# Kernel tuning notes

Measured on AMD Instinct MI355X. Metric: run time of the kernel, lower is better.

The kernel has to match this reference:

```python
import jax, jax.numpy as jnp
import numpy as np

B, L0, L1, NS, D, H, NL, HM = 16, 512, 256, 32, 256, 8, 4, 4
T = L0 + L1 + NS + 1
HD = D // H
EPS = 1e-5
SCALE = HD ** -0.5


def setup_inputs() -> dict:
    key = jax.random.key(0)
    ks = jax.random.split(key, 20)
    s = 0.02
    return {
        'seq_tokens_0': jax.random.normal(ks[0], (B, L0, D), jnp.float32),
        'seq_tokens_1': jax.random.normal(ks[1], (B, L1, D), jnp.float32),
        'seq_lens_0': jax.random.randint(ks[2], (B,), 0, L0),
        'seq_lens_1': jax.random.randint(ks[3], (B,), 0, L1),
        'ns_tokens': jax.random.normal(ks[4], (B, NS, D), jnp.float32),
        'domain_emb': jax.random.normal(ks[5], (2, D), jnp.float32) * s,
        'cls_token': jax.random.normal(ks[6], (1, 1, D), jnp.float32) * s,
        'ln1_w': jnp.ones((NL, D), jnp.float32),
        'ln1_b': jnp.zeros((NL, D), jnp.float32),
        'qkv_w': jax.random.normal(ks[7], (NL, D, 3 * D), jnp.float32) * s,
        'qkv_b': jnp.zeros((NL, 3 * D), jnp.float32),
        'out_w': jax.random.normal(ks[8], (NL, D, D), jnp.float32) * s,
        'out_b': jnp.zeros((NL, D), jnp.float32),
        'ln2_w': jnp.ones((NL, D), jnp.float32),
        'ln2_b': jnp.zeros((NL, D), jnp.float32),
        'ffn1_w': jax.random.normal(ks[9], (NL, D, HM * D), jnp.float32) * s,
        'ffn1_b': jnp.zeros((NL, HM * D), jnp.float32),
        'ffn2_w': jax.random.normal(ks[10], (NL, HM * D, D), jnp.float32) * s,
        'ffn2_b': jnp.zeros((NL, D), jnp.float32),
        'fln_w': jnp.ones((D,), jnp.float32),
        'fln_b': jnp.zeros((D,), jnp.float32),
    }


def _ln(x, w, b):
    m = jnp.mean(x, -1, keepdims=True)
    v = jnp.var(x, -1, keepdims=True)
    return (x - m) * jax.lax.rsqrt(v + EPS) * w + b


def _build_mask(seq_lens_0, seq_lens_1):
    # static block structure: intra-domain causal, S<->NS bidirectional, CLS sink row
    base = jnp.zeros((T, T), bool)
    base = base.at[:L0, :L0].set(jnp.tril(jnp.ones((L0, L0), bool)))
    base = base.at[L0:L0 + L1, L0:L0 + L1].set(jnp.tril(jnp.ones((L1, L1), bool)))
    ns_s, ns_e = L0 + L1, L0 + L1 + NS
    base = base.at[:ns_s, ns_s:ns_e].set(True)   # S -> NS
    base = base.at[ns_s:ns_e, :ns_e].set(True)   # NS -> S and NS -> NS
    base = base.at[T - 1, :ns_e].set(True)       # CLS reads all S/NS
    base = base.at[T - 1, T - 1].set(True)       # CLS reads itself
    # per-batch padding mask on keys of each seq segment
    kv = jnp.ones((B, T), bool)
    kv = kv.at[:, :L0].set(jnp.arange(L0)[None, :] < seq_lens_0[:, None])
    kv = kv.at[:, L0:L0 + L1].set(jnp.arange(L1)[None, :] < seq_lens_1[:, None])
    return base[None] & kv[:, None, :]  # [B, T, T]


def _attention(x, mask, qkv_w, qkv_b, out_w, out_b):
    qkv = (x @ qkv_w + qkv_b).reshape(B, T, 3, H, HD)
    q, k, v = qkv[:, :, 0], qkv[:, :, 1], qkv[:, :, 2]
    scores = jnp.einsum('bqhd,bkhd->bhqk', q, k) * SCALE
    m = mask[:, None]  # [B,1,T,T]
    s = jnp.where(m, scores, -jnp.inf)
    any_valid = jnp.any(m, -1, keepdims=True)
    mx = jnp.where(any_valid, jnp.max(s, -1, keepdims=True), 0.0)
    e = jnp.exp(s - mx)  # masked entries exp(-inf)=0
    denom = jnp.sum(e, -1, keepdims=True)
    probs = e / jnp.maximum(denom, 1e-30)  # fully-masked rows -> zeros
    out = jnp.einsum('bhqk,bkhd->bqhd', probs, v).reshape(B, T, D)
    return out @ out_w + out_b


def reference(seq_tokens_0, seq_tokens_1, seq_lens_0, seq_lens_1, ns_tokens,
              domain_emb, cls_token, ln1_w, ln1_b, qkv_w, qkv_b, out_w, out_b,
              ln2_w, ln2_b, ffn1_w, ffn1_b, ffn2_w, ffn2_b, fln_w, fln_b):
    t0 = seq_tokens_0 + domain_emb[0][None, None, :]
    t1 = seq_tokens_1 + domain_emb[1][None, None, :]
    cls = jnp.broadcast_to(cls_token, (B, 1, D))
    x = jnp.concatenate([t0, t1, ns_tokens, cls], axis=1)  # [B,T,D]
    mask = _build_mask(seq_lens_0, seq_lens_1)
    for l in range(NL):
        x = x + _attention(_ln(x, ln1_w[l], ln1_b[l]), mask,
                           qkv_w[l], qkv_b[l], out_w[l], out_b[l])
        h = _ln(x, ln2_w[l], ln2_b[l])
        h = jax.nn.gelu(h @ ffn1_w[l] + ffn1_b[l], approximate=False)
        x = x + h @ ffn2_w[l] + ffn2_b[l]
    x = _ln(x, fln_w, fln_b)
    return x[:, -1, :]  # CLS state [B,D]
```

## Files before the change

kernel.cpp:

```cpp
#include <hip/hip_runtime.h>
#include <hip/hip_bf16.h>
#include <math.h>

typedef __attribute__((ext_vector_type(8))) unsigned short ushort8;
typedef __attribute__((ext_vector_type(8))) short short8;
typedef __attribute__((ext_vector_type(4))) float f32x4;
typedef __attribute__((ext_vector_type(4))) unsigned short ushort4v;
typedef __attribute__((ext_vector_type(4))) int i32x4;
typedef unsigned int u32;

namespace {
constexpr int B = 16, L0 = 512, L1 = 256, NS = 32, D = 256, H = 8, NL = 4, HM = 4;
constexpr int T = L0 + L1 + NS + 1;
constexpr int HD = D / H;
constexpr int NTOK = B * T;
constexpr int NS_S = L0 + L1;
constexpr int NS_E = NS_S + NS;
constexpr int TPAD = 832;
constexpr float EPS = 1e-5f;
constexpr float SCL2  = 0.17677669529663687f * 1.4426950408889634f;
}

__device__ __forceinline__ ushort f2bf(float f) {
    union { float f; unsigned u; } v; v.f = f;
    return (ushort)((v.u + 0x7fffu + ((v.u >> 16) & 1u)) >> 16);
}

__device__ __forceinline__ u32 cvtpk(float a, float b) {
    u32 r;
    asm("v_cvt_pk_bf16_f32 %0, %1, %2" : "=v"(r) : "v"(a), "v"(b));
    return r;
}

__device__ __forceinline__ void gload_lds16(const void* g, void* l) {
    __builtin_amdgcn_global_load_lds(
        (const __attribute__((address_space(1))) u32*)g,
        (__attribute__((address_space(3))) u32*)l, 16, 0, 0);
}

__global__ __launch_bounds__(256) void k_wprep(
    const float* __restrict__ src, ushort* __restrict__ dst, int K, int N)
{
    const size_t off = (size_t)blockIdx.z * K * N;
    src += off; dst += off;
    __shared__ float t[32][33];
    const int kb = blockIdx.x * 32, nb = blockIdx.y * 32;
    const int c = threadIdx.x & 31, r8 = threadIdx.x >> 5;
#pragma unroll
    for (int rr = 0; rr < 32; rr += 8)
        t[r8 + rr][c] = src[(size_t)(kb + r8 + rr) * N + nb + c];
    __syncthreads();
#pragma unroll
    for (int rr = 0; rr < 32; rr += 8)
        dst[(size_t)(nb + r8 + rr) * K + kb + c] = f2bf(t[c][r8 + rr]);
}

__global__ __launch_bounds__(256) void k_build_ln(
    const float* __restrict__ s0, const float* __restrict__ s1,
    const float* __restrict__ ns, const float* __restrict__ dom,
    const float* __restrict__ cls, const float* __restrict__ lnw,
    const float* __restrict__ lnb, float* __restrict__ x, ushort* __restrict__ xn)
{
    const int wid = threadIdx.x >> 6, lane = threadIdx.x & 63;
    const int row = blockIdx.x * 4 + wid;
    if (row >= NTOK) return;
    const int b = row / T, t = row % T;
    const int d0 = lane * 4;
    float4 v;
    if (t < L0) {
        v = *(const float4*)(s0 + ((size_t)b * L0 + t) * D + d0);
        float4 dm = *(const float4*)(dom + d0);
        v.x += dm.x; v.y += dm.y; v.z += dm.z; v.w += dm.w;
    } else if (t < NS_S) {
        v = *(const float4*)(s1 + ((size_t)b * L1 + (t - L0)) * D + d0);
        float4 dm = *(const float4*)(dom + D + d0);
        v.x += dm.x; v.y += dm.y; v.z += dm.z; v.w += dm.w;
    } else if (t < NS_E) {
        v = *(const float4*)(ns + ((size_t)b * NS + (t - NS_S)) * D + d0);
    } else {
        v = *(const float4*)(cls + d0);
    }
    *(float4*)(x + (size_t)row * D + d0) = v;
    float s  = v.x + v.y + v.z + v.w;
    float ss = v.x * v.x + v.y * v.y + v.z * v.z + v.w * v.w;
#pragma unroll
    for (int o = 32; o; o >>= 1) { s += __shfl_xor(s, o); ss += __shfl_xor(ss, o); }
    const float mean = s * (1.f / D);
    const float var  = ss * (1.f / D) - mean * mean;
    const float r = rsqrtf(var + EPS);
    float4 wv = *(const float4*)(lnw + d0);
    float4 bv = *(const float4*)(lnb + d0);
    ushort4v o4;
    o4[0] = f2bf((v.x - mean) * r * wv.x + bv.x);
    o4[1] = f2bf((v.y - mean) * r * wv.y + bv.y);
    o4[2] = f2bf((v.z - mean) * r * wv.z + bv.z);
    o4[3] = f2bf((v.w - mean) * r * wv.w + bv.w);
    *(ushort4v*)(xn + (size_t)row * D + d0) = o4;
}

template<bool GELU, bool RES, bool OBF, bool CLSW>
__global__ __launch_bounds__(256) void k_gemm_mfma(
    const ushort* __restrict__ A, const ushort* __restrict__ Wt,
    const float* __restrict__ bias, void* __restrict__ Cout,
    const float* __restrict__ res, int M, int N, int K)
{
    __shared__ ushort As[2][128 * 64];
    __shared__ ushort Bs[2][128 * 64];
    const int tid = threadIdx.x;
    const int lane = tid & 63, w = tid >> 6;
    const int lo = lane & 15, g = lane >> 4;
    const int wr = w >> 1, wc = w & 1;
    const int m0 = CLSW ? (((blockIdx.x * T + (T - 1)) >> 7) << 7) : blockIdx.x * 128;
    const int n0 = blockIdx.y * 128;

    f32x4 zero = {0.f, 0.f, 0.f, 0.f};
    f32x4 acc[4][4];
#pragma unroll
    for (int mi = 0; mi < 4; ++mi)
#pragma unroll
        for (int ni = 0; ni < 4; ++ni) acc[mi][ni] = zero;

    const ushort* srcA[4];
    const ushort* srcB[4];
    int ldsOff[4];
#pragma unroll
    for (int i = 0; i < 4; ++i) {
        const int idx16 = (w * 4 + i) * 64 + lane;
        const int row = idx16 >> 3;
        const int scb = ((idx16 & 7) * 16) ^ ((row & 7) << 4);
        int arow = m0 + row; if (arow >= M) arow = M - 1;
        srcA[i] = A  + (size_t)arow * K + (scb >> 1);
        srcB[i] = Wt + (size_t)(n0 + row) * K + (scb >> 1);
        ldsOff[i] = (w * 4 + i) * 512;
    }

    const int NT = K >> 6;
#pragma unroll
    for (int i = 0; i < 4; ++i) {
        gload_lds16(srcA[i], &As[0][ldsOff[i]]);
        gload_lds16(srcB[i], &Bs[0][ldsOff[i]]);
    }
    asm volatile("s_waitcnt vmcnt(0)");
    __syncthreads();

    for (int t = 0; t < NT; ++t) {
        const int buf = t & 1;
        if (t + 1 < NT) {
            const int nb = buf ^ 1, ko = (t + 1) * 64;
#pragma unroll
            for (int i = 0; i < 4; ++i) {
                gload_lds16(srcA[i] + ko, &As[nb][ldsOff[i]]);
                gload_lds16(srcB[i] + ko, &Bs[nb][ldsOff[i]]);
            }
        }
#pragma unroll
        for (int kk = 0; kk < 2; ++kk) {
            const int kb = (kk * 64 + g * 16) ^ ((lo & 7) << 4);
            short8 af[4], bfr[4];
#pragma unroll
            for (int mi = 0; mi < 4; ++mi)
                af[mi] = *(const short8*)&As[buf][(wr * 64 + mi * 16 + lo) * 64 + (kb >> 1)];
#pragma unroll
            for (int ni = 0; ni < 4; ++ni)
                bfr[ni] = *(const short8*)&Bs[buf][(wc * 64 + ni * 16 + lo) * 64 + (kb >> 1)];
#pragma unroll
            for (int mi = 0; mi < 4; ++mi)
#pragma unroll
                for (int ni = 0; ni < 4; ++ni)
                    acc[mi][ni] = __builtin_amdgcn_mfma_f32_16x16x32_bf16(
                        af[mi], bfr[ni], acc[mi][ni], 0, 0, 0);
        }
        asm volatile("s_waitcnt vmcnt(0)");
        __syncthreads();
    }

    float bv[4];
#pragma unroll
    for (int ni = 0; ni < 4; ++ni) bv[ni] = bias[n0 + wc * 64 + ni * 16 + lo];
#pragma unroll
    for (int mi = 0; mi < 4; ++mi) {
#pragma unroll
        for (int i = 0; i < 4; ++i) {
            const int row = m0 + wr * 64 + mi * 16 + g * 4 + i;
            if (row >= M) continue;
#pragma unroll
            for (int ni = 0; ni < 4; ++ni) {
                const int col = n0 + wc * 64 + ni * 16 + lo;
                float v = acc[mi][ni][i] + bv[ni];
                if (GELU) v = 0.5f * v * (1.0f + erff(v * 0.70710678118654752f));
                if (RES)  v += res[(size_t)row * N + col];
                if (OBF) ((ushort*)Cout)[(size_t)row * N + col] = f2bf(v);
                else     ((float*)Cout)[(size_t)row * N + col] = v;
            }
        }
    }
}

template<int MODE, bool CLSW>
__global__ __launch_bounds__(256) void k_gemm_fused(
    const ushort* __restrict__ A, const ushort* __restrict__ Wt,
    const float* __restrict__ bias, const float* __restrict__ res,
    const float* __restrict__ lnw, const float* __restrict__ lnb,
    float* __restrict__ xout, ushort* __restrict__ xnout,
    float* __restrict__ dout, int M, int K)
{
    __shared__ ushort As[2][64 * 64];
    __shared__ ushort Bs[2][256 * 64];
    __shared__ float redS[64][4];
    __shared__ float redQ[64][4];
    const int tid = threadIdx.x;
    const int lane = tid & 63, w = tid >> 6;
    const int lo = lane & 15, g = lane >> 4;
    const int m0 = CLSW ? (((blockIdx.x * T + (T - 1)) >> 6) << 6) : blockIdx.x * 64;

    f32x4 zero = {0.f, 0.f, 0.f, 0.f};
    f32x4 acc[4][4];
#pragma unroll
    for (int mi = 0; mi < 4; ++mi)
#pragma unroll
        for (int ni = 0; ni < 4; ++ni) acc[mi][ni] = zero;

    const ushort* srcA[2]; int ldsOffA[2];
    const ushort* srcB[8]; int ldsOffB[8];
#pragma unroll
    for (int j = 0; j < 2; ++j) {
        const int idx16 = j * 256 + tid;
        const int row = idx16 >> 3;
        const int scb = ((idx16 & 7) * 16) ^ ((row & 7) << 4);
        int arow = m0 + row; if (arow >= M) arow = M - 1;
        srcA[j] = A + (size_t)arow * K + (scb >> 1);
        ldsOffA[j] = idx16 * 8;
    }
#pragma unroll
    for (int j = 0; j < 8; ++j) {
        const int idx16 = j * 256 + tid;
        const int row = idx16 >> 3;
        const int scb = ((idx16 & 7) * 16) ^ ((row & 7) << 4);
        srcB[j] = Wt + (size_t)row * K + (scb >> 1);
        ldsOffB[j] = idx16 * 8;
    }

    const int NT = K >> 6;
#pragma unroll
    for (int j = 0; j < 2; ++j) gload_lds16(srcA[j], &As[0][ldsOffA[j]]);
#pragma unroll
    for (int j = 0; j < 8; ++j) gload_lds16(srcB[j], &Bs[0][ldsOffB[j]]);
    asm volatile("s_waitcnt vmcnt(0)");
    __syncthreads();

    for (int t = 0; t < NT; ++t) {
        const int buf = t & 1;
        if (t + 1 < NT) {
            const int nb = buf ^ 1, ko = (t + 1) * 64;
#pragma unroll
            for (int j = 0; j < 2; ++j) gload_lds16(srcA[j] + ko, &As[nb][ldsOffA[j]]);
#pragma unroll
            for (int j = 0; j < 8; ++j) gload_lds16(srcB[j] + ko, &Bs[nb][ldsOffB[j]]);
        }
#pragma unroll
        for (int kk = 0; kk < 2; ++kk) {
            const int kb = (kk * 64 + g * 16) ^ ((lo & 7) << 4);
            short8 af[4], bfr[4];
#pragma unroll
            for (int mi = 0; mi < 4; ++mi)
                af[mi] = *(const short8*)&As[buf][(mi * 16 + lo) * 64 + (kb >> 1)];
#pragma unroll
            for (int ni = 0; ni < 4; ++ni)
                bfr[ni] = *(const short8*)&Bs[buf][(w * 64 + ni * 16 + lo) * 64 + (kb >> 1)];
#pragma unroll
            for (int mi = 0; mi < 4; ++mi)
#pragma unroll
                for (int ni = 0; ni < 4; ++ni)
                    acc[mi][ni] = __builtin_amdgcn_mfma_f32_16x16x32_bf16(
                        af[mi], bfr[ni], acc[mi][ni], 0, 0, 0);
        }
        asm volatile("s_waitcnt vmcnt(0)");
        __syncthreads();
    }

    float bv[4], lw[4], lb[4];
#pragma unroll
    for (int ni = 0; ni < 4; ++ni) {
        const int c = w * 64 + ni * 16 + lo;
        bv[ni] = bias[c]; lw[ni] = lnw[c]; lb[ni] = lnb[c];
    }
#pragma unroll
    for (int mi = 0; mi < 4; ++mi) {
#pragma unroll
        for (int i = 0; i < 4; ++i) {
            const int r64 = mi * 16 + g * 4 + i;
            const int row = m0 + r64;
            float s = 0.f, q = 0.f;
            if (row < M) {
#pragma unroll
                for (int ni = 0; ni < 4; ++ni) {
                    const int col = w * 64 + ni * 16 + lo;
                    float v = acc[mi][ni][i] + bv[ni] + res[(size_t)row * 256 + col];
                    acc[mi][ni][i] = v;
                    s += v; q += v * v;
                }
                s += __shfl_xor(s, 1); q += __shfl_xor(q, 1);
                s += __shfl_xor(s, 2); q += __shfl_xor(q, 2);
                s += __shfl_xor(s, 4); q += __shfl_xor(q, 4);
                s += __shfl_xor(s, 8); q += __shfl_xor(q, 8);
                if (lo == 0) { redS[r64][w] = s; redQ[r64][w] = q; }
            }
        }
    }
    __syncthreads();
#pragma unroll
    for (int mi = 0; mi < 4; ++mi) {
#pragma unroll
        for (int i = 0; i < 4; ++i) {
            const int r64 = mi * 16 + g * 4 + i;
            const int row = m0 + r64;
            if (row >= M) continue;
            const float S = redS[r64][0] + redS[r64][1] + redS[r64][2] + redS[r64][3];
            const float Q = redQ[r64][0] + redQ[r64][1] + redQ[r64][2] + redQ[r64][3];
            const float mean = S * (1.f / 256.f);
            const float var  = Q * (1.f / 256.f) - mean * mean;
            const float rstd = rsqrtf(var + EPS);
            if (MODE == 0) {
#pragma unroll
                for (int ni = 0; ni < 4; ++ni) {
                    const int col = w * 64 + ni * 16 + lo;
                    const float v = acc[mi][ni][i];
                    xout[(size_t)row * 256 + col] = v;
                    xnout[(size_t)row * 256 + col] = f2bf((v - mean) * rstd * lw[ni] + lb[ni]);
                }
            } else {
                const int bq = row / T;
                const int tq = row - bq * T;
                if (tq == T - 1) {
#pragma unroll
                    for (int ni = 0; ni < 4; ++ni) {
                        const int col = w * 64 + ni * 16 + lo;
                        dout[(size_t)bq * 256 + col] =
                            (acc[mi][ni][i] - mean) * rstd * lw[ni] + lb[ni];
                    }
                }
            }
        }
    }
}

__global__ __launch_bounds__(256) void k_repack(
    const ushort* __restrict__ qkv, ushort* __restrict__ Kb, ushort* __restrict__ Vt)
{
    const int bh = blockIdx.x, tt = blockIdx.y;
    const int b = bh >> 3, h = bh & 7;
    const int tid = threadIdx.x;
    const int r = tid >> 2, c = tid & 3;
    const int t = tt * 64 + r;
    __shared__ ushort vtile[64][40];
    ushort8 k8 = {0,0,0,0,0,0,0,0}, v8 = {0,0,0,0,0,0,0,0};
    if (t < T) {
        const ushort* kp = qkv + ((size_t)(b * T + t) * 3 + 1) * D + h * HD + c * 8;
        k8 = *(const ushort8*)kp;
        v8 = *(const ushort8*)(kp + D);
    }
    *(ushort8*)(Kb + ((size_t)bh * TPAD + tt * 64 + r) * HD + c * 8) = k8;
    *(ushort8*)&vtile[r][c * 8] = v8;
    __syncthreads();
    const int d = tid >> 3, cc = tid & 7;
    ushort8 o;
#pragma unroll
    for (int j = 0; j < 8; ++j) o[j] = vtile[cc * 8 + j][d];
    *(ushort8*)(Vt + ((size_t)bh * HD + d) * TPAD + tt * 64 + cc * 8) = o;
}

__global__ __launch_bounds__(256) void k_flash(
    const ushort* __restrict__ qkv, const ushort* __restrict__ Kb,
    const ushort* __restrict__ Vt, const int* __restrict__ len0,
    const int* __restrict__ len1, ushort* __restrict__ out)
{
    const int bh = blockIdx.x;
    const int qt = 12 - blockIdx.y;
    const int b = bh >> 3, h = bh & 7;
    const int tid = threadIdx.x, lane = tid & 63, w = tid >> 6;
    const int lo = lane & 15, g = lane >> 4;
    const int b4 = g & 1, b5 = g >> 1;
    const int q = qt * 64 + w * 16 + lo;
    const int l0b = len0[b], lim01 = L0 + len1[b];

    int klo = 0, klim;
    if (q < L0)        klim = q;
    else if (q < NS_S) { klo = L0; klim = q; }
    else if (q < NS_E) klim = NS_E - 1;
    else               klim = q;

    int qrow = q; if (qrow > T - 1) qrow = T - 1;
    short8 qf = *(const short8*)(qkv + ((size_t)(b * T + qrow) * 3) * D + h * HD + g * 8);

    const ushort* Kbase = Kb + (size_t)bh * TPAD * HD;
    const ushort* Vbase = Vt + (size_t)bh * HD * TPAD;

    f32x4 acc0 = {0.f, 0.f, 0.f, 0.f}, acc1 = {0.f, 0.f, 0.f, 0.f};
    float mrow = -1e30f, srow = 0.f;

    const int kts = (qt >= 8 && qt < 12) ? 8 : 0;
    const int ntiles = (qt < 12) ? (qt - kts + 2) : 13;
    auto ktile = [&](int it) { int kt = kts + it; return kt > qt ? 12 : kt; };

    short8 kf[4];
    {
        const int k0 = ktile(0) * 64;
#pragma unroll
        for (int n = 0; n < 4; ++n)
            kf[n] = *(const short8*)(Kbase + (size_t)(k0 + n * 16 + lo) * HD + g * 8);
    }

    for (int it = 0; it < ntiles; ++it) {
        const int k0 = ktile(it) * 64;

        const ushort* V0 = Vbase + k0;
        short8 a00 = *(const short8*)(V0 + (size_t)lo * TPAD + g * 8);
        short8 a01 = *(const short8*)(V0 + (size_t)lo * TPAD + 32 + g * 8);
        short8 a10 = *(const short8*)(V0 + (size_t)(16 + lo) * TPAD + g * 8);
        short8 a11 = *(const short8*)(V0 + (size_t)(16 + lo) * TPAD + 32 + g * 8);

        float pv[4][4];
        float tmax = -1e30f;
#pragma unroll
        for (int n = 0; n < 4; ++n) {
            f32x4 z = {0.f, 0.f, 0.f, 0.f};
            f32x4 sn = __builtin_amdgcn_mfma_f32_16x16x32_bf16(kf[n], qf, z, 0, 0, 0);
#pragma unroll
            for (int i = 0; i < 4; ++i) {
                const int k = k0 + n * 16 + g * 4 + i;
                const bool inNS = (k >= NS_S) & (k < NS_E);
                const bool kval = (k < l0b) | ((k >= L0) & (k < lim01)) | (k >= NS_S);
                const bool m = ((k >= klo) & (k <= klim) & kval) | inNS;
                const float sv = m ? sn[i] * SCL2 : -1e30f;
                pv[n][i] = sv;
                tmax = fmaxf(tmax, sv);
            }
        }

        short8 kf2[4];
        if (it + 1 < ntiles) {
            const int k1 = ktile(it + 1) * 64;
#pragma unroll
            for (int n = 0; n < 4; ++n)
                kf2[n] = *(const short8*)(Kbase + (size_t)(k1 + n * 16 + lo) * HD + g * 8);
        }

        tmax = fmaxf(tmax, __shfl_xor(tmax, 16));
        tmax = fmaxf(tmax, __shfl_xor(tmax, 32));
        const float mnew = fmaxf(mrow, tmax);
        const float scl = exp2f(mrow - mnew);
        mrow = mnew;

        u32 C0[4], C1[4];
        float psum = 0.f;
#pragma unroll
        for (int n = 0; n < 4; ++n) {
            float e0 = exp2f(pv[n][0] - mnew);
            float e1 = exp2f(pv[n][1] - mnew);
            float e2 = exp2f(pv[n][2] - mnew);
            float e3 = exp2f(pv[n][3] - mnew);
            psum += (e0 + e1) + (e2 + e3);
            C0[n] = cvtpk(e0, e1);
            C1[n] = cvtpk(e2, e3);
        }
        psum += __shfl_xor(psum, 16);
        psum += __shfl_xor(psum, 32);
        srow = srow * scl + psum;
#pragma unroll
        for (int i = 0; i < 4; ++i) { acc0[i] *= scl; acc1[i] *= scl; }

        u32 pb0u[4], pb1u[4];
#pragma unroll
        for (int n = 0; n < 4; ++n) {
            const u32 F0 = (u32)__shfl_xor((int)C0[n], 16);
            const u32 F1 = (u32)__shfl_xor((int)C1[n], 16);
            const u32 G00 = b4 ? F0 : C0[n];
            const u32 G01 = b4 ? C0[n] : F0;
            const u32 G10 = b4 ? F1 : C1[n];
            const u32 G11 = b4 ? C1[n] : F1;
            const u32 H00 = (u32)__shfl_xor((int)G00, 32);
            const u32 H01 = (u32)__shfl_xor((int)G01, 32);
            const u32 H10 = (u32)__shfl_xor((int)G10, 32);
            const u32 H11 = (u32)__shfl_xor((int)G11, 32);
            const bool keep = (b5 == b4);
            const u32 S00 = keep ? G00 : H00;
            const u32 S01 = keep ? G01 : H01;
            const u32 S10 = keep ? G10 : H10;
            const u32 S11 = keep ? G11 : H11;
            const bool take = (b5 == (n & 1));
            if ((n >> 1) == 0) {
                pb0u[0] = take ? S00 : pb0u[0];
                pb0u[1] = take ? S10 : pb0u[1];
                pb0u[2] = take ? S01 : pb0u[2];
                pb0u[3] = take ? S11 : pb0u[3];
            } else {
                pb1u[0] = take ? S00 : pb1u[0];
                pb1u[1] = take ? S10 : pb1u[1];
                pb1u[2] = take ? S01 : pb1u[2];
                pb1u[3] = take ? S11 : pb1u[3];
            }
        }
        i32x4 t0 = { (int)pb0u[0], (int)pb0u[1], (int)pb0u[2], (int)pb0u[3] };
        i32x4 t1 = { (int)pb1u[0], (int)pb1u[1], (int)pb1u[2], (int)pb1u[3] };
        const short8 pb0 = __builtin_bit_cast(short8, t0);
        const short8 pb1 = __builtin_bit_cast(short8, t1);

        acc0 = __builtin_amdgcn_mfma_f32_16x16x32_bf16(a00, pb0, acc0, 0, 0, 0);
        acc0 = __builtin_amdgcn_mfma_f32_16x16x32_bf16(a01, pb1, acc0, 0, 0, 0);
        acc1 = __builtin_amdgcn_mfma_f32_16x16x32_bf16(a10, pb0, acc1, 0, 0, 0);
        acc1 = __builtin_amdgcn_mfma_f32_16x16x32_bf16(a11, pb1, acc1, 0, 0, 0);

#pragma unroll
        for (int n = 0; n < 4; ++n) kf[n] = kf2[n];
    }

    if (q < T) {
        const float inv = 1.f / fmaxf(srow, 1e-30f);
        ushort* orow = out + (size_t)(b * T + q) * D + h * HD;
        *(u32*)(orow + g * 4)          = cvtpk(acc0[0] * inv, acc0[1] * inv);
        *(u32*)(orow + g * 4 + 2)      = cvtpk(acc0[2] * inv, acc0[3] * inv);
        *(u32*)(orow + 16 + g * 4)     = cvtpk(acc1[0] * inv, acc1[1] * inv);
        *(u32*)(orow + 16 + g * 4 + 2) = cvtpk(acc1[2] * inv, acc1[3] * inv);
    }
}

extern "C" void kernel_launch(void* const* d_in, const int* in_sizes, int n_in,
                              void* d_out, int out_size, void* d_ws, size_t ws_size,
                              hipStream_t stream)
{
    const float* seq0 = (const float*)d_in[0];
    const float* seq1 = (const float*)d_in[1];
    const int*   len0 = (const int*)d_in[2];
    const int*   len1 = (const int*)d_in[3];
    const float* nst  = (const float*)d_in[4];
    const float* dom  = (const float*)d_in[5];
    const float* cls  = (const float*)d_in[6];
    const float* ln1w = (const float*)d_in[7];
    const float* ln1b = (const float*)d_in[8];
    const float* qkvw = (const float*)d_in[9];
    const float* qkvb = (const float*)d_in[10];
    const float* outw = (const float*)d_in[11];
    const float* outb = (const float*)d_in[12];
    const float* ln2w = (const float*)d_in[13];
    const float* ln2b = (const float*)d_in[14];
    const float* f1w  = (const float*)d_in[15];
    const float* f1b  = (const float*)d_in[16];
    const float* f2w  = (const float*)d_in[17];
    const float* f2b  = (const float*)d_in[18];
    const float* flnw = (const float*)d_in[19];
    const float* flnb = (const float*)d_in[20];

    float*  x   = (float*)d_ws;
    ushort* xn  = (ushort*)(x + (size_t)NTOK * D);
    ushort* big = xn + (size_t)NTOK * D;
    ushort* Kb  = big + (size_t)NTOK * HM * D;
    ushort* Vt  = Kb + (size_t)B * H * TPAD * HD;
    ushort* qkvw_t = Vt + (size_t)B * H * TPAD * HD;
    ushort* outw_t = qkvw_t + (size_t)NL * 768 * 256;
    ushort* f1w_t  = outw_t + (size_t)NL * 256 * 256;
    ushort* f2w_t  = f1w_t  + (size_t)NL * 1024 * 256;

    k_wprep<<<dim3(256 / 32, 768 / 32, NL), 256, 0, stream>>>(qkvw, qkvw_t, 256, 768);
    k_wprep<<<dim3(256 / 32, 256 / 32, NL), 256, 0, stream>>>(outw, outw_t, 256, 256);
    k_wprep<<<dim3(256 / 32, 1024 / 32, NL), 256, 0, stream>>>(f1w, f1w_t, 256, 1024);
    k_wprep<<<dim3(1024 / 32, 256 / 32, NL), 256, 0, stream>>>(f2w, f2w_t, 1024, 256);

    k_build_ln<<<(NTOK + 3) / 4, 256, 0, stream>>>(seq0, seq1, nst, dom, cls,
                                                   ln1w, ln1b, x, xn);

    const int gmm = (NTOK + 127) / 128;
    const int gf  = (NTOK + 63) / 64;

    for (int l = 0; l < NL; ++l) {
        const bool last = (l == NL - 1);
        k_gemm_mfma<false, false, true, false><<<dim3(gmm, 6), 256, 0, stream>>>(
            xn, qkvw_t + (size_t)l * 768 * 256, qkvb + (size_t)l * 3 * D, big, nullptr,
            NTOK, 3 * D, D);
        k_repack<<<dim3(B * H, TPAD / 64), 256, 0, stream>>>(big, Kb, Vt);
        k_flash<<<dim3(B * H, last ? 1 : TPAD / 64), 256, 0, stream>>>(
            big, Kb, Vt, len0, len1, xn);
        if (!last)
            k_gemm_fused<0, false><<<gf, 256, 0, stream>>>(
                xn, outw_t + (size_t)l * 256 * 256, outb + (size_t)l * D, x,
                ln2w + l * D, ln2b + l * D, x, xn, nullptr, NTOK, D);
        else
            k_gemm_fused<0, true><<<B, 256, 0, stream>>>(
                xn, outw_t + (size_t)l * 256 * 256, outb + (size_t)l * D, x,
                ln2w + l * D, ln2b + l * D, x, xn, nullptr, NTOK, D);
        if (!last)
            k_gemm_mfma<true, false, true, false><<<dim3(gmm, 8), 256, 0, stream>>>(
                xn, f1w_t + (size_t)l * 1024 * 256, f1b + (size_t)l * HM * D, big,
                nullptr, NTOK, HM * D, D);
        else
            k_gemm_mfma<true, false, true, true><<<dim3(B, 8), 256, 0, stream>>>(
                xn, f1w_t + (size_t)l * 1024 * 256, f1b + (size_t)l * HM * D, big,
                nullptr, NTOK, HM * D, D);
        if (!last)
            k_gemm_fused<0, false><<<gf, 256, 0, stream>>>(
                big, f2w_t + (size_t)l * 256 * 1024, f2b + (size_t)l * D, x,
                ln1w + (l + 1) * D, ln1b + (l + 1) * D, x, xn, nullptr, NTOK, HM * D);
        else
            k_gemm_fused<1, true><<<B, 256, 0, stream>>>(
                big, f2w_t + (size_t)l * 256 * 1024, f2b + (size_t)l * D, x,
                flnw, flnb, nullptr, nullptr, (float*)d_out, NTOK, HM * D);
    }
}
```

Baseline: 537.9 us.

## Skip padded sequence tokens in GEMMs, repack and flash attention

Adds a per-block check against the sequence lengths so that GEMM, repack and flash-attention blocks covering only padded token positions exit early. The flash kernel also limits its key-tile loop to tiles that hold valid keys for each domain. Padded tokens cannot influence the CLS output through the mask, so their activations are left stale instead of recomputed. This removes roughly half the token work, since lengths are uniform random, at the cost of a few scalar length loads per block.

```diff
diff --git a/kernel.cpp b/kernel.cpp
--- a/kernel.cpp
+++ b/kernel.cpp
@@ -36,6 +36,21 @@
     __builtin_amdgcn_global_load_lds(
         (const __attribute__((address_space(1))) u32*)g,
         (__attribute__((address_space(3))) u32*)l, 16, 0, 0);
+}
+
+__device__ __forceinline__ bool any_valid_rows(
+    int m0, int rows, const int* __restrict__ len0, const int* __restrict__ len1)
+{
+    int m1 = m0 + rows; if (m1 > NTOK) m1 = NTOK;
+    const int b0 = m0 / T, b1 = (m1 - 1) / T;
+    for (int b = b0; b <= b1; ++b) {
+        int t0 = m0 - b * T; if (t0 < 0) t0 = 0;
+        int t1 = m1 - b * T; if (t1 > T) t1 = T;
+        if (t0 < len0[b]) return true;
+        if (t1 > L0 && t0 < L0 + len1[b]) return true;
+        if (t1 > NS_S) return true;
+    }
+    return false;
 }
 
 __global__ __launch_bounds__(256) void k_wprep(
@@ -102,7 +117,8 @@
 __global__ __launch_bounds__(256) void k_gemm_mfma(
     const ushort* __restrict__ A, const ushort* __restrict__ Wt,
     const float* __restrict__ bias, void* __restrict__ Cout,
-    const float* __restrict__ res, int M, int N, int K)
+    const float* __restrict__ res, const int* __restrict__ len0,
+    const int* __restrict__ len1, int M, int N, int K)
 {
     __shared__ ushort As[2][128 * 64];
     __shared__ ushort Bs[2][128 * 64];
@@ -113,6 +129,8 @@
     const int m0 = CLSW ? (((blockIdx.x * T + (T - 1)) >> 7) << 7) : blockIdx.x * 128;
     const int n0 = blockIdx.y * 128;
 
+    if (!CLSW && !any_valid_rows(m0, 128, len0, len1)) return;
+
     f32x4 zero = {0.f, 0.f, 0.f, 0.f};
     f32x4 acc[4][4];
 #pragma unroll
@@ -202,7 +220,8 @@
     const float* __restrict__ bias, const float* __restrict__ res,
     const float* __restrict__ lnw, const float* __restrict__ lnb,
     float* __restrict__ xout, ushort* __restrict__ xnout,
-    float* __restrict__ dout, int M, int K)
+    float* __restrict__ dout, const int* __restrict__ len0,
+    const int* __restrict__ len1, int M, int K)
 {
     __shared__ ushort As[2][64 * 64];
     __shared__ ushort Bs[2][256 * 64];
@@ -212,6 +231,8 @@
     const int lane = tid & 63, w = tid >> 6;
     const int lo = lane & 15, g = lane >> 4;
     const int m0 = CLSW ? (((blockIdx.x * T + (T - 1)) >> 6) << 6) : blockIdx.x * 64;
+
+    if (!CLSW && !any_valid_rows(m0, 64, len0, len1)) return;
 
     f32x4 zero = {0.f, 0.f, 0.f, 0.f};
     f32x4 acc[4][4];
@@ -345,13 +366,17 @@
 }
 
 __global__ __launch_bounds__(256) void k_repack(
-    const ushort* __restrict__ qkv, ushort* __restrict__ Kb, ushort* __restrict__ Vt)
+    const ushort* __restrict__ qkv, ushort* __restrict__ Kb, ushort* __restrict__ Vt,
+    const int* __restrict__ len0, const int* __restrict__ len1)
 {
     const int bh = blockIdx.x, tt = blockIdx.y;
     const int b = bh >> 3, h = bh & 7;
+    const int t0 = tt * 64;
+    if (tt < 8)       { if (t0 >= len0[b]) return; }
+    else if (tt < 12) { if (t0 >= L0 + len1[b]) return; }
     const int tid = threadIdx.x;
     const int r = tid >> 2, c = tid & 3;
-    const int t = tt * 64 + r;
+    const int t = t0 + r;
     __shared__ ushort vtile[64][40];
     ushort8 k8 = {0,0,0,0,0,0,0,0}, v8 = {0,0,0,0,0,0,0,0};
     if (t < T) {
@@ -359,14 +384,14 @@
         k8 = *(const ushort8*)kp;
         v8 = *(const ushort8*)(kp + D);
     }
-    *(ushort8*)(Kb + ((size_t)bh * TPAD + tt * 64 + r) * HD + c * 8) = k8;
+    *(ushort8*)(Kb + ((size_t)bh * TPAD + t0 + r) * HD + c * 8) = k8;
     *(ushort8*)&vtile[r][c * 8] = v8;
     __syncthreads();
     const int d = tid >> 3, cc = tid & 7;
     ushort8 o;
 #pragma unroll
     for (int j = 0; j < 8; ++j) o[j] = vtile[cc * 8 + j][d];
-    *(ushort8*)(Vt + ((size_t)bh * HD + d) * TPAD + tt * 64 + cc * 8) = o;
+    *(ushort8*)(Vt + ((size_t)bh * HD + d) * TPAD + t0 + cc * 8) = o;
 }
 
 __global__ __launch_bounds__(256) void k_flash(
@@ -377,11 +402,16 @@
     const int bh = blockIdx.x;
     const int qt = 12 - blockIdx.y;
     const int b = bh >> 3, h = bh & 7;
+    const int l0b = len0[b], lim01 = L0 + len1[b];
+
+    const int q0t = qt * 64;
+    if (qt < 8)       { if (q0t >= l0b) return; }
+    else if (qt < 12) { if (q0t >= lim01) return; }
+
     const int tid = threadIdx.x, lane = tid & 63, w = tid >> 6;
     const int lo = lane & 15, g = lane >> 4;
     const int b4 = g & 1, b5 = g >> 1;
-    const int q = qt * 64 + w * 16 + lo;
-    const int l0b = len0[b], lim01 = L0 + len1[b];
+    const int q = q0t + w * 16 + lo;
 
     int klo = 0, klim;
     if (q < L0)        klim = q;
@@ -398,9 +428,14 @@
     f32x4 acc0 = {0.f, 0.f, 0.f, 0.f}, acc1 = {0.f, 0.f, 0.f, 0.f};
     float mrow = -1e30f, srow = 0.f;
 
-    const int kts = (qt >= 8 && qt < 12) ? 8 : 0;
-    const int ntiles = (qt < 12) ? (qt - kts + 2) : 13;
-    auto ktile = [&](int it) { int kt = kts + it; return kt > qt ? 12 : kt; };
+    const int lt0 = (l0b + 63) >> 6;
+    const int lt1 = (lim01 - L0 + 63) >> 6;
+    int nc0, nc1;
+    if (qt < 8)       { nc0 = min(qt + 1, lt0); nc1 = 0; }
+    else if (qt < 12) { nc0 = 0; nc1 = min(qt - 7, lt1); }
+    else              { nc0 = lt0; nc1 = lt1; }
+    const int ntiles = nc0 + nc1 + 1;
+    auto ktile = [&](int it) { return (it < nc0) ? it : (it < nc0 + nc1) ? (8 + it - nc0) : 12; };
 
     short8 kf[4];
     {
@@ -575,33 +610,34 @@
         const bool last = (l == NL - 1);
         k_gemm_mfma<false, false, true, false><<<dim3(gmm, 6), 256, 0, stream>>>(
             xn, qkvw_t + (size_t)l * 768 * 256, qkvb + (size_t)l * 3 * D, big, nullptr,
-            NTOK, 3 * D, D);
-        k_repack<<<dim3(B * H, TPAD / 64), 256, 0, stream>>>(big, Kb, Vt);
+            len0, len1, NTOK, 3 * D, D);
+        k_repack<<<dim3(B * H, TPAD / 64), 256, 0, stream>>>(big, Kb, Vt, len0, len1);
         k_flash<<<dim3(B * H, last ? 1 : TPAD / 64), 256, 0, stream>>>(
             big, Kb, Vt, len0, len1, xn);
         if (!last)
             k_gemm_fused<0, false><<<gf, 256, 0, stream>>>(
                 xn, outw_t + (size_t)l * 256 * 256, outb + (size_t)l * D, x,
-                ln2w + l * D, ln2b + l * D, x, xn, nullptr, NTOK, D);
+                ln2w + l * D, ln2b + l * D, x, xn, nullptr, len0, len1, NTOK, D);
         else
             k_gemm_fused<0, true><<<B, 256, 0, stream>>>(
                 xn, outw_t + (size_t)l * 256 * 256, outb + (size_t)l * D, x,
-                ln2w + l * D, ln2b + l * D, x, xn, nullptr, NTOK, D);
+                ln2w + l * D, ln2b + l * D, x, xn, nullptr, len0, len1, NTOK, D);
         if (!last)
             k_gemm_mfma<true, false, true, false><<<dim3(gmm, 8), 256, 0, stream>>>(
                 xn, f1w_t + (size_t)l * 1024 * 256, f1b + (size_t)l * HM * D, big,
-                nullptr, NTOK, HM * D, D);
+                nullptr, len0, len1, NTOK, HM * D, D);
         else
             k_gemm_mfma<true, false, true, true><<<dim3(B, 8), 256, 0, stream>>>(
                 xn, f1w_t + (size_t)l * 1024 * 256, f1b + (size_t)l * HM * D, big,
-                nullptr, NTOK, HM * D, D);
+                nullptr, len0, len1, NTOK, HM * D, D);
         if (!last)
             k_gemm_fused<0, false><<<gf, 256, 0, stream>>>(
                 big, f2w_t + (size_t)l * 256 * 1024, f2b + (size_t)l * D, x,
-                ln1w + (l + 1) * D, ln1b + (l + 1) * D, x, xn, nullptr, NTOK, HM * D);
+                ln1w + (l + 1) * D, ln1b + (l + 1) * D, x, xn, nullptr, len0, len1,
+                NTOK, HM * D);
         else
             k_gemm_fused<1, true><<<B, 256, 0, stream>>>(
                 big, f2w_t + (size_t)l * 256 * 1024, f2b + (size_t)l * D, x,
-                flnw, flnb, nullptr, nullptr, (float*)d_out, NTOK, HM * D);
-    }
-}
+                flnw, flnb, nullptr, nullptr, (float*)d_out, len0, len1, NTOK, HM * D);
+    }
+}
```

Result: faster. 478.1 us (-11.1%).
